# Optimization experiments

Measured on AMD Instinct MI355X. Metric: run time of the kernel, lower is better.

## Reference

```python
import jax, jax.numpy as jnp
import numpy as np

EMBED_DIM = 1024
NUM_HEADS = 16
HEAD_DIM = EMBED_DIM // NUM_HEADS


def _rope_tables(seq_len, dim, dtype):
    # inv_freq over even indices of head_dim
    inv_freq = 1.0 / (10000.0 ** (jnp.arange(0, dim, 2, dtype=jnp.float32) / dim))
    t = jnp.arange(seq_len, dtype=jnp.float32)
    freqs = jnp.einsum('i,j->ij', t, inv_freq)            # [S, dim/2]
    emb = jnp.concatenate([freqs, freqs], axis=-1)        # [S, dim]
    return jnp.cos(emb).astype(dtype)[None], jnp.sin(emb).astype(dtype)[None]  # [1,S,dim]


def _rotate_half(x):
    x1, x2 = jnp.split(x, 2, axis=-1)
    return jnp.concatenate([-x2, x1], axis=-1)


def _apply_rope(x, cos, sin):
    return x * cos + _rotate_half(x) * sin


def setup_inputs() -> dict:
    key = jax.random.key(0)
    ks = jax.random.split(key, 9)
    S, B, E = 2048, 2, EMBED_DIM
    sc = 1.0 / np.sqrt(E)
    inp = {
        'query': jax.random.normal(ks[0], (S, B, E), jnp.float32),
        'Wq': jax.random.normal(ks[1], (E, E), jnp.float32) * sc,
        'bq': jnp.zeros((E,), jnp.float32),
        'Wk': jax.random.normal(ks[2], (E, E), jnp.float32) * sc,
        'bk': jnp.zeros((E,), jnp.float32),
        'Wv': jax.random.normal(ks[3], (E, E), jnp.float32) * sc,
        'bv': jnp.zeros((E,), jnp.float32),
        'Wo': jax.random.normal(ks[4], (E, E), jnp.float32) * sc,
        'bo': jnp.zeros((E,), jnp.float32),
    }
    return inp


def reference(query, Wq, bq, Wk, bk, Wv, bv, Wo, bo):
    tgt_len, bsz, E = query.shape
    H, hd = NUM_HEADS, HEAD_DIM
    scaling = hd ** (-0.5)

    # self-attention projections (torch Linear: x @ W.T + b)
    q = (query @ Wq.T + bq) * scaling
    k = query @ Wk.T + bk
    v = query @ Wv.T + bv

    # [S, B, E] -> [B*H, S, hd]
    def to_heads(x):
        return x.reshape(tgt_len, bsz * H, hd).transpose(1, 0, 2)

    q, k, v = to_heads(q), to_heads(k), to_heads(v)

    cos, sin = _rope_tables(tgt_len, hd, q.dtype)  # [1,S,hd]
    q = _apply_rope(q, cos, sin)
    k = _apply_rope(k, cos, sin)

    attn_weights = jnp.einsum('bqd,bkd->bqk', q, k)       # [B*H, S, S]
    attn_probs = jax.nn.softmax(attn_weights, axis=-1)
    attn = jnp.einsum('bqk,bkd->bqd', attn_probs, v)      # [B*H, S, hd]

    attn = attn.transpose(1, 0, 2).reshape(tgt_len, bsz, E)
    return attn @ Wo.T + bo
```

## Files before the change

### kernel.cpp

```cpp
#include <hip/hip_runtime.h>
#include <hip/hip_bf16.h>


typedef short shortx8 __attribute__((ext_vector_type(8)));
typedef float floatx4 __attribute__((ext_vector_type(4)));
typedef float floatx16 __attribute__((ext_vector_type(16)));

#define S_LEN 2048
#define BATCH 2
#define EMB 1024
#define NH 16
#define HD 64
#define BH 32
#define MROWS 4096
#define HEAD_STRIDE (S_LEN*HD)

#define QSCALE 0.1803368801111204f

#if __has_builtin(__builtin_amdgcn_exp2f)
#define EXP2(x) __builtin_amdgcn_exp2f(x)
#else
#define EXP2(x) exp2f(x)
#endif

__device__ __forceinline__ float b2f(unsigned short u) {
    union { unsigned int i; float f; } v; v.i = ((unsigned int)u) << 16; return v.f;
}
__device__ __forceinline__ unsigned short f2b(float f) {
    union { float f; unsigned int i; } v; v.f = f;
    unsigned int x = v.i;
    return (unsigned short)((x + 0x7fffu + ((x >> 16) & 1u)) >> 16);
}
__device__ __forceinline__ unsigned short f2b_fast(float f) {
    union { float f; unsigned int i; } v; v.f = f;
    return (unsigned short)((v.i + 0x8000u) >> 16);
}
__device__ __forceinline__ unsigned int fbits(float f) {
    union { float f; unsigned int i; } v; v.f = f; return v.i;
}
__device__ __forceinline__ unsigned int pack_bf16_2(float lo, float hi) {
    return __builtin_amdgcn_perm(fbits(hi) + 0x8000u, fbits(lo) + 0x8000u, 0x07060302u);
}
__device__ __forceinline__ unsigned int cvtpk_bf16(float lo, float hi) {
    unsigned int r;
    asm("v_cvt_pk_bf16_f32 %0, %1, %2" : "=v"(r) : "v"(lo), "v"(hi));
    return r;
}
__device__ __forceinline__ void plswap(unsigned int &a, unsigned int &b) {
#if __has_builtin(__builtin_amdgcn_permlane32_swap)
    {
        auto r = __builtin_amdgcn_permlane32_swap(a, b, false, false);
        a = r[0]; b = r[1];
    }
#else
    asm volatile("v_permlane32_swap_b32 %0, %1" : "+v"(a), "+v"(b));
#endif
}
__device__ __forceinline__ shortx8 cvt8(const float* p) {
    floatx4 a = *(const floatx4*)p;
    floatx4 b = *(const floatx4*)(p + 4);
    shortx8 r;
    r[0] = (short)f2b(a[0]); r[1] = (short)f2b(a[1]);
    r[2] = (short)f2b(a[2]); r[3] = (short)f2b(a[3]);
    r[4] = (short)f2b(b[0]); r[5] = (short)f2b(b[1]);
    r[6] = (short)f2b(b[2]); r[7] = (short)f2b(b[3]);
    return r;
}
__device__ __forceinline__ shortx8 cvt8f(const float* p) {
    floatx4 a = *(const floatx4*)p;
    floatx4 b = *(const floatx4*)(p + 4);
    union { uint4 u; shortx8 s; } r;
    r.u.x = pack_bf16_2(a[0], a[1]);
    r.u.y = pack_bf16_2(a[2], a[3]);
    r.u.z = pack_bf16_2(b[0], b[1]);
    r.u.w = pack_bf16_2(b[2], b[3]);
    return r.s;
}
__device__ __forceinline__ void g2l16(const unsigned short* g, unsigned short* l) {
    __builtin_amdgcn_global_load_lds(
        (const __attribute__((address_space(1))) unsigned int*)(const void*)g,
        (__attribute__((address_space(3))) unsigned int*)(void*)l, 16, 0, 0);
}

__global__ __launch_bounds__(256) void prep(
    const float* __restrict__ X,
    const float* __restrict__ Wq, const float* __restrict__ Wk,
    const float* __restrict__ Wv,
    unsigned short* __restrict__ Xb, unsigned short* __restrict__ Wb,
    float* __restrict__ rtab)
{
    const int g = blockIdx.x * 256 + threadIdx.x;
    if (g < 65536) {
        const int s = g >> 5, j = g & 31;
        const float inv = expf(-(float)j * (9.210340371976184f / 32.0f));
        const float ang = (float)s * inv;
        rtab[s * 64 + j]      = cosf(ang);
        rtab[s * 64 + 32 + j] = sinf(ang);
    } else if (g < 458752) {
        const int h = g - 65536;
        const int seg = h >> 17;
        const int idx = (h & 131071) * 8;
        const float* W = (seg == 0) ? Wq : (seg == 1) ? Wk : Wv;
        *(shortx8*)&Wb[seg * 1048576 + idx] = cvt8(&W[idx]);
    } else {
        const int idx = (g - 458752) * 8;
        *(shortx8*)&Xb[idx] = cvt8(&X[idx]);
    }
}

__device__ __forceinline__ void qkv_epilogue(
    floatx4 (&acc)[4][4], int mat, int m0, int nn0, int wm, int wn,
    int qm, int quad, const float* bias, const float* rtab,
    unsigned short* dst)
{
    if (mat == 2) {
#pragma unroll
        for (int i = 0; i < 4; i++) {
#pragma unroll
            for (int j = 0; j < 4; j++) {
                const int colg = nn0 + wn + j * 16 + qm;
                const float bv_ = bias[colg];
                const int h = colg >> 6, d = colg & 63;
#pragma unroll
                for (int r = 0; r < 4; r++) {
                    const int rowg = m0 + wm + i * 16 + quad * 4 + r;
                    const int s = rowg >> 1, b = rowg & 1;
                    dst[((b * NH + h) * HD + d) * S_LEN + s] = f2b(acc[i][j][r] + bv_);
                }
            }
        }
    } else {
        const float scale = (mat == 0) ? QSCALE : 1.0f;
#pragma unroll
        for (int i = 0; i < 4; i++) {
#pragma unroll
            for (int jp = 0; jp < 2; jp++) {
                const int c1 = nn0 + wn + jp * 16 + qm;
                const float b1 = bias[c1], b2 = bias[c1 + 32];
                const int h = c1 >> 6;
                const int d1 = c1 & 63;
#pragma unroll
                for (int r = 0; r < 4; r++) {
                    const int rowg = m0 + wm + i * 16 + quad * 4 + r;
                    const int s = rowg >> 1, b = rowg & 1;
                    const float cs = rtab[s * 64 + d1];
                    const float sn = rtab[s * 64 + d1 + 32];
                    const float x1 = (acc[i][jp][r] + b1) * scale;
                    const float x2 = (acc[i][jp + 2][r] + b2) * scale;
                    unsigned short* base = &dst[((b * NH + h) * S_LEN + s) * HD];
                    base[d1]      = f2b(x1 * cs - x2 * sn);
                    base[d1 + 32] = f2b(x2 * cs + x1 * sn);
                }
            }
        }
    }
}

__global__ __launch_bounds__(256) void qkv_gemm_gl(
    const unsigned short* __restrict__ Xb,
    const unsigned short* __restrict__ Wb,
    const float* __restrict__ bq, const float* __restrict__ bk,
    const float* __restrict__ bv,
    const float* __restrict__ rtab,
    unsigned short* __restrict__ Qh, unsigned short* __restrict__ Kh,
    unsigned short* __restrict__ Vt)
{
    __shared__ unsigned short At[128 * 64];
    __shared__ unsigned short Bt[128 * 64];

    const int tid  = threadIdx.x;
    const int wave = tid >> 6, lane = tid & 63;
    const int wm = (wave >> 1) * 64, wn = (wave & 1) * 64;
    const int qm = lane & 15, quad = lane >> 4;

    const int m0  = blockIdx.x * 128;
    const int n0g = blockIdx.y * 128;
    const int mat = n0g >> 10;
    const int nn0 = n0g & 1023;

    const unsigned short* W = Wb + (size_t)mat * 1048576;
    const float* bias = (mat == 0) ? bq : (mat == 1) ? bk : bv;
    unsigned short* dst = (mat == 0) ? Qh : (mat == 1) ? Kh : Vt;

    floatx4 acc[4][4] = {};

    const int xs = qm & 7;

    for (int k0 = 0; k0 < EMB; k0 += 64) {
#pragma unroll
        for (int c = 0; c < 4; c++) {
            const int e   = (c * 256 + tid) * 8;
            const int row = e >> 6;
            const int gcol = (((e >> 3) & 7) ^ (row & 7)) * 8;
            g2l16(&Xb[(m0 + row) * EMB + k0 + gcol], &At[e]);
            g2l16(&W[(nn0 + row) * EMB + k0 + gcol], &Bt[e]);
        }
        __syncthreads();

#pragma unroll
        for (int kk = 0; kk < 2; kk++) {
            shortx8 a[4], b[4];
#pragma unroll
            for (int i = 0; i < 4; i++)
                a[i] = *(shortx8*)&At[(wm + i * 16 + qm) * 64 + (((kk * 4 + quad) ^ xs) * 8)];
#pragma unroll
            for (int j = 0; j < 4; j++)
                b[j] = *(shortx8*)&Bt[(wn + j * 16 + qm) * 64 + (((kk * 4 + quad) ^ xs) * 8)];
#pragma unroll
            for (int i = 0; i < 4; i++)
#pragma unroll
                for (int j = 0; j < 4; j++)
                    acc[i][j] = __builtin_amdgcn_mfma_f32_16x16x32_bf16(a[i], b[j], acc[i][j], 0, 0, 0);
        }
        __syncthreads();
    }

    qkv_epilogue(acc, mat, m0, nn0, wm, wn, qm, quad, bias, rtab, dst);
}

#define LDB 72

__global__ __launch_bounds__(256) void qkv_gemm_fb(
    const float* __restrict__ X,
    const unsigned short* __restrict__ Wb,
    const float* __restrict__ bq, const float* __restrict__ bk,
    const float* __restrict__ bv,
    const float* __restrict__ rtab,
    unsigned short* __restrict__ Qh, unsigned short* __restrict__ Kh,
    unsigned short* __restrict__ Vt)
{
    __shared__ unsigned short At[128 * LDB];
    __shared__ unsigned short Bt[128 * LDB];

    const int tid  = threadIdx.x;
    const int wave = tid >> 6, lane = tid & 63;
    const int wm = (wave >> 1) * 64, wn = (wave & 1) * 64;
    const int qm = lane & 15, quad = lane >> 4;

    const int m0  = blockIdx.x * 128;
    const int n0g = blockIdx.y * 128;
    const int mat = n0g >> 10;
    const int nn0 = n0g & 1023;

    const unsigned short* W = Wb + (size_t)mat * 1048576;
    const float* bias = (mat == 0) ? bq : (mat == 1) ? bk : bv;
    unsigned short* dst = (mat == 0) ? Qh : (mat == 1) ? Kh : Vt;

    const int r0 = tid >> 3;
    const int ko = (tid & 7) * 8;

    floatx4 acc[4][4] = {};

    for (int k0 = 0; k0 < EMB; k0 += 64) {
#pragma unroll
        for (int c = 0; c < 4; c++) {
            const int row = r0 + 32 * c;
            *(shortx8*)&At[row * LDB + ko] = cvt8(&X[(m0 + row) * EMB + k0 + ko]);
            *(shortx8*)&Bt[row * LDB + ko] = *(const shortx8*)&W[(nn0 + row) * EMB + k0 + ko];
        }
        __syncthreads();

#pragma unroll
        for (int kk = 0; kk < 2; kk++) {
            shortx8 a[4], b[4];
#pragma unroll
            for (int i = 0; i < 4; i++)
                a[i] = *(shortx8*)&At[(wm + i * 16 + qm) * LDB + kk * 32 + quad * 8];
#pragma unroll
            for (int j = 0; j < 4; j++)
                b[j] = *(shortx8*)&Bt[(wn + j * 16 + qm) * LDB + kk * 32 + quad * 8];
#pragma unroll
            for (int i = 0; i < 4; i++)
#pragma unroll
                for (int j = 0; j < 4; j++)
                    acc[i][j] = __builtin_amdgcn_mfma_f32_16x16x32_bf16(a[i], b[j], acc[i][j], 0, 0, 0);
        }
        __syncthreads();
    }

    qkv_epilogue(acc, mat, m0, nn0, wm, wn, qm, quad, bias, rtab, dst);
}

#define SW8(c8, r) ((((c8) ^ ((r) & 7))) * 8)

__global__ __launch_bounds__(512, 4) void attn_kernel(
    unsigned short* Qh,
    const unsigned short* __restrict__ Kh,
    const unsigned short* __restrict__ Vt)
{
    __shared__ __align__(16) unsigned short lds[8192 + 8192 + 512];
    unsigned short* ldsK  = lds;
    unsigned short* ldsVT = lds + 8192;

    const int tid  = threadIdx.x;
    const int wave = tid >> 6, lane = tid & 63;
    const int l32 = lane & 31, half = lane >> 5;
    const int qg = wave >> 1, ks = wave & 1;
    const int bh = blockIdx.y;
    const int qrow = blockIdx.x * 128 + qg * 32;

    unsigned short* Qp = Qh + bh * HEAD_STRIDE;
    const unsigned short* Kp = Kh + bh * HEAD_STRIDE;
    const unsigned short* Vp = Vt + bh * HEAD_STRIDE;

    shortx8 aq[4];
#pragma unroll
    for (int kk = 0; kk < 4; kk++)
        aq[kk] = *(const shortx8*)&Qp[(qrow + l32) * HD + kk * 16 + half * 8];

    floatx16 od0 = {}, od1 = {};
    float l_run = 0.0f;

    const int kb = ks * 64;

    const int kr = tid >> 3, kc8 = tid & 7;
    const int vr = tid >> 4, vc8 = tid & 15;

    for (int kt = 0; kt < S_LEN / 128; kt++) {
        const int kbase = kt * 128;
        *(shortx8*)&ldsK[kr * 64 + SW8(kc8, kr)] =
            *(const shortx8*)&Kp[(kbase + kr) * HD + kc8 * 8];
        *(shortx8*)&ldsK[(kr + 64) * 64 + SW8(kc8, kr)] =
            *(const shortx8*)&Kp[(kbase + kr + 64) * HD + kc8 * 8];
        *(shortx8*)&ldsVT[vr * 128 + SW8(vc8, vr)] =
            *(const shortx8*)&Vp[vr * S_LEN + kbase + vc8 * 8];
        *(shortx8*)&ldsVT[(vr + 32) * 128 + SW8(vc8, vr)] =
            *(const shortx8*)&Vp[(vr + 32) * S_LEN + kbase + vc8 * 8];
        __syncthreads();

#pragma unroll
        for (int sub = 0; sub < 2; sub++) {
            floatx16 sc = {};
#pragma unroll
            for (int kk = 0; kk < 4; kk++) {
                const shortx8 kf = *(shortx8*)&ldsK[
                    (kb + sub * 32 + l32) * 64 + SW8(kk * 2 + half, l32)];
                sc = __builtin_amdgcn_mfma_f32_32x32x16_bf16(kf, aq[kk], sc, 0, 0, 0);
            }
            float p[16];
#pragma unroll
            for (int g = 0; g < 16; g++) p[g] = EXP2(sc[g]);
#pragma unroll
            for (int c = 0; c < 4; c++)
                l_run += (p[4 * c] + p[4 * c + 1]) + (p[4 * c + 2] + p[4 * c + 3]);

#pragma unroll
            for (int f = 0; f < 2; f++) {
                unsigned int d0 = cvtpk_bf16(p[8 * f + 0], p[8 * f + 1]);
                unsigned int d2 = cvtpk_bf16(p[8 * f + 4], p[8 * f + 5]);
                plswap(d0, d2);
                unsigned int d1 = cvtpk_bf16(p[8 * f + 2], p[8 * f + 3]);
                unsigned int d3 = cvtpk_bf16(p[8 * f + 6], p[8 * f + 7]);
                plswap(d1, d3);
                union { unsigned int u[4]; shortx8 s; } fr;
                fr.u[0] = d0; fr.u[1] = d1; fr.u[2] = d2; fr.u[3] = d3;

                const int c8 = (kb >> 3) + (sub * 2 + f) * 2 + half;
                const shortx8 v0 = *(shortx8*)&ldsVT[l32 * 128 + SW8(c8, l32)];
                const shortx8 v1 = *(shortx8*)&ldsVT[(32 + l32) * 128 + SW8(c8, l32)];
                od0 = __builtin_amdgcn_mfma_f32_32x32x16_bf16(fr.s, v0, od0, 0, 0, 0);
                od1 = __builtin_amdgcn_mfma_f32_32x32x16_bf16(fr.s, v1, od1, 0, 0, 0);
            }
        }
        __syncthreads();
    }

    l_run += __shfl_xor(l_run, 32, 64);

    float* ltab  = (float*)(lds + 16384) + qg * 64 + ks * 32;
    float* odbuf = (float*)lds + qg * 2048;
    if (half == 0) ltab[l32] = l_run;
    if (ks == 1) {
#pragma unroll
        for (int g = 0; g < 16; g++) {
            const int row = (g & 3) + 8 * (g >> 2) + 4 * half;
            odbuf[row * 64 + l32]      = od0[g];
            odbuf[row * 64 + 32 + l32] = od1[g];
        }
    }
    __syncthreads();
    if (ks == 0) {
        const float* l0 = (float*)(lds + 16384) + qg * 64;
        const float* l1 = l0 + 32;
#pragma unroll
        for (int g = 0; g < 16; g++) {
            const int row = (g & 3) + 8 * (g >> 2) + 4 * half;
            const float inv = 1.0f / (l0[row] + l1[row]);
            const float v0 = od0[g] + odbuf[row * 64 + l32];
            const float v1 = od1[g] + odbuf[row * 64 + 32 + l32];
            Qp[(qrow + row) * HD + l32]      = f2b(v0 * inv);
            Qp[(qrow + row) * HD + 32 + l32] = f2b(v1 * inv);
        }
    }
}

__global__ __launch_bounds__(256) void out_gemm(
    const unsigned short* __restrict__ O,
    const float* __restrict__ Wo, const float* __restrict__ bo,
    float* __restrict__ out)
{
    __shared__ unsigned short At[128 * LDB];
    __shared__ unsigned short Bt[64 * LDB];

    const int tid  = threadIdx.x;
    const int wave = tid >> 6, lane = tid & 63;
    const int wm = (wave >> 1) * 64, wn = (wave & 1) * 32;
    const int qm = lane & 15, quad = lane >> 4;
    const int m0 = blockIdx.x * 128;
    const int n0 = blockIdx.y * 64;

    const int r0 = tid >> 3;
    const int ko = (tid & 7) * 8;

    floatx4 acc[4][2] = {};

    for (int k0 = 0; k0 < EMB; k0 += 64) {
        const int k = k0 + ko;
#pragma unroll
        for (int c = 0; c < 4; c++) {
            const int row = r0 + 32 * c;
            const int m = m0 + row;
            *(shortx8*)&At[row * LDB + ko] =
                *(const shortx8*)&O[(((m & 1) * NH + (k >> 6)) * S_LEN + (m >> 1)) * HD + (k & 63)];
        }
#pragma unroll
        for (int c = 0; c < 2; c++) {
            const int row = r0 + 32 * c;
            *(shortx8*)&Bt[row * LDB + ko] = cvt8f(&Wo[(n0 + row) * EMB + k]);
        }
        __syncthreads();

#pragma unroll
        for (int kk = 0; kk < 2; kk++) {
            shortx8 a[4], b[2];
#pragma unroll
            for (int i = 0; i < 4; i++)
                a[i] = *(shortx8*)&At[(wm + i * 16 + qm) * LDB + kk * 32 + quad * 8];
#pragma unroll
            for (int j = 0; j < 2; j++)
                b[j] = *(shortx8*)&Bt[(wn + j * 16 + qm) * LDB + kk * 32 + quad * 8];
#pragma unroll
            for (int i = 0; i < 4; i++)
#pragma unroll
                for (int j = 0; j < 2; j++)
                    acc[i][j] = __builtin_amdgcn_mfma_f32_16x16x32_bf16(a[i], b[j], acc[i][j], 0, 0, 0);
        }
        __syncthreads();
    }

#pragma unroll
    for (int i = 0; i < 4; i++) {
#pragma unroll
        for (int j = 0; j < 2; j++) {
            const int colg = n0 + wn + j * 16 + qm;
            const float bv_ = bo[colg];
#pragma unroll
            for (int r = 0; r < 4; r++) {
                const int rowg = m0 + wm + i * 16 + quad * 4 + r;
                out[rowg * EMB + colg] = acc[i][j][r] + bv_;
            }
        }
    }
}

extern "C" void kernel_launch(void* const* d_in, const int* in_sizes, int n_in,
                              void* d_out, int out_size, void* d_ws, size_t ws_size,
                              hipStream_t stream) {
    const float* X  = (const float*)d_in[0];
    const float* Wq = (const float*)d_in[1];
    const float* bq = (const float*)d_in[2];
    const float* Wk = (const float*)d_in[3];
    const float* bk = (const float*)d_in[4];
    const float* Wv = (const float*)d_in[5];
    const float* bv = (const float*)d_in[6];
    const float* Wo = (const float*)d_in[7];
    const float* bo = (const float*)d_in[8];
    float* out = (float*)d_out;

    unsigned short* ws = (unsigned short*)d_ws;
    unsigned short* Vt  = ws;
    unsigned short* Qh  = ws + (size_t)BH * HEAD_STRIDE;
    unsigned short* Xb  = ws + (size_t)2 * BH * HEAD_STRIDE;
    unsigned short* Kh  = (unsigned short*)d_out;
    unsigned short* Wb  = (unsigned short*)d_out + 4194304;
    float*          Rt  = (float*)d_out + 3670016;

    const bool use_xb = ws_size >= (size_t)24 * 1024 * 1024;

    prep<<<dim3(use_xb ? 3840 : 1792), 256, 0, stream>>>(X, Wq, Wk, Wv, Xb, Wb, Rt);

    if (use_xb)
        qkv_gemm_gl<<<dim3(MROWS / 128, 3 * EMB / 128), 256, 0, stream>>>(
            Xb, Wb, bq, bk, bv, Rt, Qh, Kh, Vt);
    else
        qkv_gemm_fb<<<dim3(MROWS / 128, 3 * EMB / 128), 256, 0, stream>>>(
            X, Wb, bq, bk, bv, Rt, Qh, Kh, Vt);

    attn_kernel<<<dim3(S_LEN / 128, BH), 512, 0, stream>>>(Qh, Kh, Vt);
    out_gemm<<<dim3(MROWS / 128, EMB / 64), 256, 0, stream>>>(Qh, Wo, bo, out);
}
```

Baseline: 200.9 us.

## Rewrite QKV GEMM as 256x256 tile, 8-wave double-buffered pipelined kernel

Replaces the 128x128, 4-wave QKV projection GEMM with a 256x256-tile, 512-thread kernel. It double-buffers LDS with direct global-to-LDS loads, overlaps the next K-slice prefetch with MFMA work using raw barriers and vmcnt waits, and raises wave priority around the MFMA blocks. The larger tile improves operand reuse and cuts global traffic, and the pipeline hides load latency. The cost is a 128KB LDS footprint, fewer blocks (192), more accumulator registers per wave, and hand-managed synchronisation that is fragile.

New measurement: 211.1 us. 1.05x slower.

```diff
diff --git a/kernel.cpp b/kernel.cpp
--- a/kernel.cpp
+++ b/kernel.cpp
@@ -30,10 +30,6 @@
     union { float f; unsigned int i; } v; v.f = f;
     unsigned int x = v.i;
     return (unsigned short)((x + 0x7fffu + ((x >> 16) & 1u)) >> 16);
-}
-__device__ __forceinline__ unsigned short f2b_fast(float f) {
-    union { float f; unsigned int i; } v; v.f = f;
-    return (unsigned short)((v.i + 0x8000u) >> 16);
 }
 __device__ __forceinline__ unsigned int fbits(float f) {
     union { float f; unsigned int i; } v; v.f = f; return v.i;
@@ -81,6 +77,10 @@
         (const __attribute__((address_space(1))) unsigned int*)(const void*)g,
         (__attribute__((address_space(3))) unsigned int*)(void*)l, 16, 0, 0);
 }
+
+#define RAW_BAR() asm volatile("s_barrier" ::: "memory")
+#define WAITVM4() asm volatile("s_waitcnt vmcnt(4)" ::: "memory")
+#define WAITVM0() asm volatile("s_waitcnt vmcnt(0)" ::: "memory")
 
 __global__ __launch_bounds__(256) void prep(
     const float* __restrict__ X,
@@ -108,55 +108,7 @@
     }
 }
 
-__device__ __forceinline__ void qkv_epilogue(
-    floatx4 (&acc)[4][4], int mat, int m0, int nn0, int wm, int wn,
-    int qm, int quad, const float* bias, const float* rtab,
-    unsigned short* dst)
-{
-    if (mat == 2) {
-#pragma unroll
-        for (int i = 0; i < 4; i++) {
-#pragma unroll
-            for (int j = 0; j < 4; j++) {
-                const int colg = nn0 + wn + j * 16 + qm;
-                const float bv_ = bias[colg];
-                const int h = colg >> 6, d = colg & 63;
-#pragma unroll
-                for (int r = 0; r < 4; r++) {
-                    const int rowg = m0 + wm + i * 16 + quad * 4 + r;
-                    const int s = rowg >> 1, b = rowg & 1;
-                    dst[((b * NH + h) * HD + d) * S_LEN + s] = f2b(acc[i][j][r] + bv_);
-                }
-            }
-        }
-    } else {
-        const float scale = (mat == 0) ? QSCALE : 1.0f;
-#pragma unroll
-        for (int i = 0; i < 4; i++) {
-#pragma unroll
-            for (int jp = 0; jp < 2; jp++) {
-                const int c1 = nn0 + wn + jp * 16 + qm;
-                const float b1 = bias[c1], b2 = bias[c1 + 32];
-                const int h = c1 >> 6;
-                const int d1 = c1 & 63;
-#pragma unroll
-                for (int r = 0; r < 4; r++) {
-                    const int rowg = m0 + wm + i * 16 + quad * 4 + r;
-                    const int s = rowg >> 1, b = rowg & 1;
-                    const float cs = rtab[s * 64 + d1];
-                    const float sn = rtab[s * 64 + d1 + 32];
-                    const float x1 = (acc[i][jp][r] + b1) * scale;
-                    const float x2 = (acc[i][jp + 2][r] + b2) * scale;
-                    unsigned short* base = &dst[((b * NH + h) * S_LEN + s) * HD];
-                    base[d1]      = f2b(x1 * cs - x2 * sn);
-                    base[d1 + 32] = f2b(x2 * cs + x1 * sn);
-                }
-            }
-        }
-    }
-}
-
-__global__ __launch_bounds__(256) void qkv_gemm_gl(
+__global__ __launch_bounds__(512, 2) void qkv_gemm_8p(
     const unsigned short* __restrict__ Xb,
     const unsigned short* __restrict__ Wb,
     const float* __restrict__ bq, const float* __restrict__ bk,
@@ -165,16 +117,15 @@
     unsigned short* __restrict__ Qh, unsigned short* __restrict__ Kh,
     unsigned short* __restrict__ Vt)
 {
-    __shared__ unsigned short At[128 * 64];
-    __shared__ unsigned short Bt[128 * 64];
+    __shared__ unsigned short sm[65536];
 
     const int tid  = threadIdx.x;
     const int wave = tid >> 6, lane = tid & 63;
-    const int wm = (wave >> 1) * 64, wn = (wave & 1) * 64;
+    const int wr = wave >> 2, wc = wave & 3;
     const int qm = lane & 15, quad = lane >> 4;
 
-    const int m0  = blockIdx.x * 128;
-    const int n0g = blockIdx.y * 128;
+    const int m0  = blockIdx.x * 256;
+    const int n0g = blockIdx.y * 256;
     const int mat = n0g >> 10;
     const int nn0 = n0g & 1023;
 
@@ -182,40 +133,148 @@
     const float* bias = (mat == 0) ? bq : (mat == 1) ? bk : bv;
     unsigned short* dst = (mat == 0) ? Qh : (mat == 1) ? Kh : Vt;
 
-    floatx4 acc[4][4] = {};
-
-    const int xs = qm & 7;
-
-    for (int k0 = 0; k0 < EMB; k0 += 64) {
-#pragma unroll
-        for (int c = 0; c < 4; c++) {
-            const int e   = (c * 256 + tid) * 8;
-            const int row = e >> 6;
-            const int gcol = (((e >> 3) & 7) ^ (row & 7)) * 8;
-            g2l16(&Xb[(m0 + row) * EMB + k0 + gcol], &At[e]);
-            g2l16(&W[(nn0 + row) * EMB + k0 + gcol], &Bt[e]);
-        }
-        __syncthreads();
-
-#pragma unroll
-        for (int kk = 0; kk < 2; kk++) {
-            shortx8 a[4], b[4];
-#pragma unroll
-            for (int i = 0; i < 4; i++)
-                a[i] = *(shortx8*)&At[(wm + i * 16 + qm) * 64 + (((kk * 4 + quad) ^ xs) * 8)];
+    const int e0 = tid * 8, e1 = 4096 + tid * 8;
+    const int r0s = e0 >> 5, r1s = e1 >> 5;
+    const int lc0 = ((((e0 >> 3) & 3) ^ ((r0s >> 1) & 3)) * 8);
+    const int lc1 = ((((e1 >> 3) & 3) ^ ((r1s >> 1) & 3)) * 8);
+    const unsigned short* gA0 = &Xb[(m0 + r0s) * EMB + lc0];
+    const unsigned short* gA1 = &Xb[(m0 + r1s) * EMB + lc1];
+    const unsigned short* gB0 = &W[(nn0 + r0s) * EMB + lc0];
+    const unsigned short* gB1 = &W[(nn0 + r1s) * EMB + lc1];
+
+    const int swz = (quad ^ ((qm >> 1) & 3)) * 8;
+    const int sAo = (wr * 128 + qm) * 32 + swz;
+    const int sBo = 16384 + (wc * 64 + qm) * 32 + swz;
+
+    floatx4 acc[8][4] = {};
+
+    g2l16(gA0, &sm[e0]);             g2l16(gA1, &sm[e1]);
+    g2l16(gB0, &sm[16384 + e0]);     g2l16(gB1, &sm[16384 + e1]);
+    g2l16(gA0 + 32, &sm[8192 + e0]); g2l16(gA1 + 32, &sm[8192 + e1]);
+    g2l16(gB0 + 32, &sm[8192 + 16384 + e0]);
+    g2l16(gB1 + 32, &sm[8192 + 16384 + e1]);
+    WAITVM4();
+    RAW_BAR();
+
+    for (int t = 0; t < 16; ++t) {
+        const int bufo = (t & 1) << 15;
+        const int nbo  = ((t + 1) & 1) << 15;
+        const bool pf  = (t + 1) < 16;
+        const int ko   = (t + 1) * 64;
+
+        shortx8 a[4], b[4];
+
+#pragma unroll
+        for (int i = 0; i < 4; i++) a[i] = *(const shortx8*)&sm[bufo + sAo + i * 512];
+#pragma unroll
+        for (int j = 0; j < 4; j++) b[j] = *(const shortx8*)&sm[bufo + sBo + j * 512];
+        if (pf) {
+            g2l16(gA0 + ko, &sm[nbo + e0]);
+            g2l16(gA1 + ko, &sm[nbo + e1]);
+            g2l16(gB0 + ko, &sm[nbo + 16384 + e0]);
+            g2l16(gB1 + ko, &sm[nbo + 16384 + e1]);
+        }
+        RAW_BAR();
+        __builtin_amdgcn_s_setprio(1);
+#pragma unroll
+        for (int i = 0; i < 4; i++)
 #pragma unroll
             for (int j = 0; j < 4; j++)
-                b[j] = *(shortx8*)&Bt[(wn + j * 16 + qm) * 64 + (((kk * 4 + quad) ^ xs) * 8)];
-#pragma unroll
-            for (int i = 0; i < 4; i++)
-#pragma unroll
-                for (int j = 0; j < 4; j++)
-                    acc[i][j] = __builtin_amdgcn_mfma_f32_16x16x32_bf16(a[i], b[j], acc[i][j], 0, 0, 0);
-        }
-        __syncthreads();
-    }
-
-    qkv_epilogue(acc, mat, m0, nn0, wm, wn, qm, quad, bias, rtab, dst);
+                acc[i][j] = __builtin_amdgcn_mfma_f32_16x16x32_bf16(a[i], b[j], acc[i][j], 0, 0, 0);
+        __builtin_amdgcn_s_setprio(0);
+        RAW_BAR();
+
+#pragma unroll
+        for (int i = 0; i < 4; i++) a[i] = *(const shortx8*)&sm[bufo + sAo + 2048 + i * 512];
+        RAW_BAR();
+        __builtin_amdgcn_s_setprio(1);
+#pragma unroll
+        for (int i = 0; i < 4; i++)
+#pragma unroll
+            for (int j = 0; j < 4; j++)
+                acc[4 + i][j] = __builtin_amdgcn_mfma_f32_16x16x32_bf16(a[i], b[j], acc[4 + i][j], 0, 0, 0);
+        __builtin_amdgcn_s_setprio(0);
+        if (pf) { WAITVM4(); } else { WAITVM0(); }
+        RAW_BAR();
+
+        {
+            const int k1 = bufo + 8192;
+#pragma unroll
+            for (int i = 0; i < 4; i++) a[i] = *(const shortx8*)&sm[k1 + sAo + i * 512];
+#pragma unroll
+            for (int j = 0; j < 4; j++) b[j] = *(const shortx8*)&sm[k1 + sBo + j * 512];
+        }
+        if (pf) {
+            g2l16(gA0 + ko + 32, &sm[nbo + 8192 + e0]);
+            g2l16(gA1 + ko + 32, &sm[nbo + 8192 + e1]);
+            g2l16(gB0 + ko + 32, &sm[nbo + 8192 + 16384 + e0]);
+            g2l16(gB1 + ko + 32, &sm[nbo + 8192 + 16384 + e1]);
+        }
+        RAW_BAR();
+        __builtin_amdgcn_s_setprio(1);
+#pragma unroll
+        for (int i = 0; i < 4; i++)
+#pragma unroll
+            for (int j = 0; j < 4; j++)
+                acc[i][j] = __builtin_amdgcn_mfma_f32_16x16x32_bf16(a[i], b[j], acc[i][j], 0, 0, 0);
+        __builtin_amdgcn_s_setprio(0);
+        RAW_BAR();
+
+#pragma unroll
+        for (int i = 0; i < 4; i++) a[i] = *(const shortx8*)&sm[bufo + 8192 + sAo + 2048 + i * 512];
+        RAW_BAR();
+        __builtin_amdgcn_s_setprio(1);
+#pragma unroll
+        for (int i = 0; i < 4; i++)
+#pragma unroll
+            for (int j = 0; j < 4; j++)
+                acc[4 + i][j] = __builtin_amdgcn_mfma_f32_16x16x32_bf16(a[i], b[j], acc[4 + i][j], 0, 0, 0);
+        __builtin_amdgcn_s_setprio(0);
+        if (pf) { WAITVM4(); }
+        RAW_BAR();
+    }
+
+    if (mat == 2) {
+#pragma unroll
+        for (int i = 0; i < 8; i++) {
+#pragma unroll
+            for (int j = 0; j < 4; j++) {
+                const int colg = nn0 + wc * 64 + j * 16 + qm;
+                const float bv_ = bias[colg];
+                const int h = colg >> 6, d = colg & 63;
+#pragma unroll
+                for (int r = 0; r < 4; r++) {
+                    const int rowg = m0 + wr * 128 + i * 16 + quad * 4 + r;
+                    const int s = rowg >> 1, bb = rowg & 1;
+                    dst[((bb * NH + h) * HD + d) * S_LEN + s] = f2b(acc[i][j][r] + bv_);
+                }
+            }
+        }
+    } else {
+        const float scale = (mat == 0) ? QSCALE : 1.0f;
+#pragma unroll
+        for (int i = 0; i < 8; i++) {
+#pragma unroll
+            for (int jp = 0; jp < 2; jp++) {
+                const int c1 = nn0 + wc * 64 + jp * 16 + qm;
+                const float b1 = bias[c1], b2 = bias[c1 + 32];
+                const int h = c1 >> 6;
+                const int d1 = jp * 16 + qm;
+#pragma unroll
+                for (int r = 0; r < 4; r++) {
+                    const int rowg = m0 + wr * 128 + i * 16 + quad * 4 + r;
+                    const int s = rowg >> 1, bb = rowg & 1;
+                    const float cs = rtab[s * 64 + d1];
+                    const float sn = rtab[s * 64 + d1 + 32];
+                    const float x1 = (acc[i][jp][r] + b1) * scale;
+                    const float x2 = (acc[i][jp + 2][r] + b2) * scale;
+                    unsigned short* base = &dst[((bb * NH + h) * S_LEN + s) * HD];
+                    base[d1]      = f2b(x1 * cs - x2 * sn);
+                    base[d1 + 32] = f2b(x2 * cs + x1 * sn);
+                }
+            }
+        }
+    }
 }
 
 #define LDB 72
@@ -278,7 +337,47 @@
         __syncthreads();
     }
 
-    qkv_epilogue(acc, mat, m0, nn0, wm, wn, qm, quad, bias, rtab, dst);
+    if (mat == 2) {
+#pragma unroll
+        for (int i = 0; i < 4; i++) {
+#pragma unroll
+            for (int j = 0; j < 4; j++) {
+                const int colg = nn0 + wn + j * 16 + qm;
+                const float bv_ = bias[colg];
+                const int h = colg >> 6, d = colg & 63;
+#pragma unroll
+                for (int r = 0; r < 4; r++) {
+                    const int rowg = m0 + wm + i * 16 + quad * 4 + r;
+                    const int s = rowg >> 1, bb = rowg & 1;
+                    dst[((bb * NH + h) * HD + d) * S_LEN + s] = f2b(acc[i][j][r] + bv_);
+                }
+            }
+        }
+    } else {
+        const float scale = (mat == 0) ? QSCALE : 1.0f;
+#pragma unroll
+        for (int i = 0; i < 4; i++) {
+#pragma unroll
+            for (int jp = 0; jp < 2; jp++) {
+                const int c1 = nn0 + wn + jp * 16 + qm;
+                const float b1 = bias[c1], b2 = bias[c1 + 32];
+                const int h = c1 >> 6;
+                const int d1 = c1 & 63;
+#pragma unroll
+                for (int r = 0; r < 4; r++) {
+                    const int rowg = m0 + wm + i * 16 + quad * 4 + r;
+                    const int s = rowg >> 1, bb = rowg & 1;
+                    const float cs = rtab[s * 64 + d1];
+                    const float sn = rtab[s * 64 + d1 + 32];
+                    const float x1 = (acc[i][jp][r] + b1) * scale;
+                    const float x2 = (acc[i][jp + 2][r] + b2) * scale;
+                    unsigned short* base = &dst[((bb * NH + h) * S_LEN + s) * HD];
+                    base[d1]      = f2b(x1 * cs - x2 * sn);
+                    base[d1 + 32] = f2b(x2 * cs + x1 * sn);
+                }
+            }
+        }
+    }
 }
 
 #define SW8(c8, r) ((((c8) ^ ((r) & 7))) * 8)
@@ -490,7 +589,7 @@
     prep<<<dim3(use_xb ? 3840 : 1792), 256, 0, stream>>>(X, Wq, Wk, Wv, Xb, Wb, Rt);
 
     if (use_xb)
-        qkv_gemm_gl<<<dim3(MROWS / 128, 3 * EMB / 128), 256, 0, stream>>>(
+        qkv_gemm_8p<<<dim3(MROWS / 256, 3 * EMB / 256), 512, 0, stream>>>(
             Xb, Wb, bq, bk, bv, Rt, Qh, Kh, Vt);
     else
         qkv_gemm_fb<<<dim3(MROWS / 128, 3 * EMB / 128), 256, 0, stream>>>(
```
